# Kernel optimization log

Hardware: AMD Instinct MI355X
Metric: run time of the kernel (lower is better)

Reference implementation:

```python
import jax, jax.numpy as jnp
import numpy as np

N = 500000
V = 50000
GF = 64
OC = 256

def _lin(key, din, dout):
    k1, k2 = jax.random.split(key)
    w = jax.random.normal(k1, (din, dout), dtype=jnp.float32) * 0.02
    b = jax.random.normal(k2, (dout,), dtype=jnp.float32) * 0.02
    return w, b

def setup_inputs() -> dict:
    key = jax.random.key(0)
    ks = jax.random.split(key, 12)
    inp_feat = jax.random.normal(ks[0], (N, 6), dtype=jnp.float32)
    vox2point_idx = jax.random.randint(ks[1], (N,), 0, V, dtype=jnp.int32)
    w1x, b1x = _lin(ks[2], 3, GF)
    w2x, b2x = _lin(ks[3], GF, OC // 8)
    w1r, b1r = _lin(ks[4], 3, GF)
    w2r, b2r = _lin(ks[5], GF, OC // 8)
    wax, bax = _lin(ks[6], OC // 4, OC // 8)
    war, bar = _lin(ks[7], OC // 4, OC // 8)
    wv1, bv1 = _lin(ks[8], OC // 2, OC // 2)
    w3, b3 = _lin(ks[9], OC, OC)
    w4, b4 = _lin(ks[10], OC, OC)
    wv2, bv2 = _lin(ks[11], OC, OC)
    return dict(inp_feat=inp_feat, vox2point_idx=vox2point_idx, num_vox=V,
                w1x=w1x, b1x=b1x, w2x=w2x, b2x=b2x,
                w1r=w1r, b1r=b1r, w2r=w2r, b2r=b2r,
                wax=wax, bax=bax, war=war, bar=bar,
                wv1=wv1, bv1=bv1, w3=w3, b3=b3, w4=w4, b4=b4,
                wv2=wv2, bv2=bv2)

def reference(inp_feat, vox2point_idx, num_vox,
              w1x, b1x, w2x, b2x, w1r, b1r, w2r, b2r,
              wax, bax, war, bar, wv1, bv1, w3, b3, w4, b4, wv2, bv2):
    relu = jax.nn.relu
    xyz = inp_feat[:, :3]
    rgb = inp_feat[:, 3:]
    fx = relu(relu(xyz @ w1x + b1x) @ w2x + b2x)   # [N, 32]
    fr = relu(relu(rgb @ w1r + b1r) @ w2r + b2r)   # [N, 32]
    comb = jnp.concatenate([fx, fr], axis=-1)       # [N, 64]
    pf2 = jnp.concatenate([
        fx, fx * jax.nn.sigmoid(comb @ wax + bax),
        fr, fr * jax.nn.sigmoid(comb @ war + bar)], axis=-1)  # [N, 128]
    # scatter-max to voxels; torch_scatter fills empty segments with 0 and
    # pf2 >= 0 elementwise, so clamp -inf (jax empty fill) to 0 for parity.
    vox = jax.ops.segment_max(pf2, vox2point_idx, num_segments=num_vox)
    vox = jnp.maximum(vox, 0.0)                     # [V, 128]
    vox = relu(vox @ wv1 + bv1)
    pg = vox[vox2point_idx]                          # gather back [N, 128]
    pf3 = jnp.concatenate([pg, pf2], axis=-1)        # [N, 256]
    pf5 = relu(relu(pf3 @ w3 + b3) @ w4 + b4)        # [N, 256]
    vox2 = jax.ops.segment_max(pf5, vox2point_idx, num_segments=num_vox)
    vox2 = jnp.maximum(vox2, 0.0)
    return relu(vox2 @ wv2 + bv2)                    # [V, 256]
```

## Files before the change

kernel.cpp:

```cpp
#include <hip/hip_runtime.h>

#define NPTS 500000
#define NVOX 50000
#define NBLK 196

typedef unsigned short u16;
typedef unsigned int u32;
typedef __attribute__((ext_vector_type(8))) short short8;
typedef __attribute__((ext_vector_type(4))) float floatx4;
typedef __attribute__((ext_vector_type(4))) unsigned int uintx4;

__device__ __forceinline__ u16 f2bf(float f) {
    u32 u = __float_as_uint(f);
    u = u + 0x7fffu + ((u >> 16) & 1u);
    return (u16)(u >> 16);
}

__global__ void k_wtransform(const float* __restrict__ W, u16* __restrict__ Wf, int K, int N) {
    int t = blockIdx.x * 256 + threadIdx.x;
    if (t >= K * N) return;
    int k = t / N, n = t - k * N;
    int kk = k >> 5, q = (k >> 3) & 3, j = k & 7;
    Wf[((size_t)((kk * 4 + q) * N + n) << 3) + j] = f2bf(W[t]);
}

__global__ void k_wcat(const float* __restrict__ w2x, const float* __restrict__ w2r, u16* __restrict__ wcatf) {
    int t = blockIdx.x * 256 + threadIdx.x;
    if (t >= 128 * 64) return;
    int k = t >> 6, n = t & 63;
    float v;
    if (k < 64) v = (n < 32) ? w2x[k * 32 + n] : 0.f;
    else        v = (n >= 32) ? w2r[(k - 64) * 32 + (n - 32)] : 0.f;
    int kk = k >> 5, q = (k >> 3) & 3, j = k & 7;
    wcatf[((size_t)((kk * 4 + q) * 64 + n) << 3) + j] = f2bf(v);
}

__global__ void k_watt(const float* __restrict__ wax, const float* __restrict__ war, u16* __restrict__ wattf) {
    int t = blockIdx.x * 256 + threadIdx.x;
    if (t >= 64 * 64) return;
    int k = t >> 6, n = t & 63;
    float v = (n < 32) ? wax[k * 32 + n] : war[k * 32 + (n - 32)];
    int kk = k >> 5, q = (k >> 3) & 3, j = k & 7;
    wattf[((size_t)((kk * 4 + q) * 64 + n) << 3) + j] = f2bf(v);
}

__global__ void k_hist(const int* __restrict__ idx, int* __restrict__ hcnt) {
    int i = blockIdx.x * 256 + threadIdx.x;
    if (i < NPTS) atomicAdd(&hcnt[idx[i]], 1);
}

__global__ __launch_bounds__(256) void k_scan1(const int* __restrict__ hcnt, int* __restrict__ bsum) {
    __shared__ int wsum[4];
    int t = threadIdx.x;
    int i = blockIdx.x * 256 + t;
    int c = (i < NVOX) ? hcnt[i] : 0;
    #pragma unroll
    for (int d = 32; d >= 1; d >>= 1) c += __shfl_xor(c, d, 64);
    if ((t & 63) == 0) wsum[t >> 6] = c;
    __syncthreads();
    if (t == 0) bsum[blockIdx.x] = wsum[0] + wsum[1] + wsum[2] + wsum[3];
}

__global__ __launch_bounds__(256) void k_scan2(const int* __restrict__ bsum, int* __restrict__ boff) {
    __shared__ int wsum[4];
    int t = threadIdx.x, lane = t & 63, w = t >> 6;
    int c = (t < NBLK) ? bsum[t] : 0;
    int v = c;
    #pragma unroll
    for (int d = 1; d < 64; d <<= 1) {
        int o = __shfl_up(v, d, 64);
        if (lane >= d) v += o;
    }
    if (lane == 63) wsum[w] = v;
    __syncthreads();
    int wo = 0;
    #pragma unroll
    for (int k = 0; k < 4; k++) if (k < w) wo += wsum[k];
    if (t < NBLK) boff[t] = wo + v - c;
}

__global__ __launch_bounds__(256) void k_scan3(const int* __restrict__ hcnt, const int* __restrict__ boff,
                                               int* __restrict__ start, int* __restrict__ cur) {
    __shared__ int wsum[4];
    int t = threadIdx.x, lane = t & 63, w = t >> 6;
    int i = blockIdx.x * 256 + t;
    int c = (i < NVOX) ? hcnt[i] : 0;
    int v = c;
    #pragma unroll
    for (int d = 1; d < 64; d <<= 1) {
        int o = __shfl_up(v, d, 64);
        if (lane >= d) v += o;
    }
    if (lane == 63) wsum[w] = v;
    __syncthreads();
    int wo = 0;
    #pragma unroll
    for (int k = 0; k < 4; k++) if (k < w) wo += wsum[k];
    if (i < NVOX) {
        int excl = boff[blockIdx.x] + wo + v - c;
        start[i] = excl;
        cur[i] = excl;
    }
}

__global__ void k_scatter(const int* __restrict__ idx, int* __restrict__ cur,
                          int* __restrict__ rank, int* __restrict__ svid) {
    int i = blockIdx.x * 256 + threadIdx.x;
    if (i < NPTS) {
        int v = idx[i];
        int pos = atomicAdd(&cur[v], 1);
        rank[i] = pos;
        svid[pos] = v;
    }
}

__global__ __launch_bounds__(256) void k_pointfeat(
    const float* __restrict__ inp, const int* __restrict__ rank,
    const float* __restrict__ w1x, const float* __restrict__ b1x,
    const float* __restrict__ w1r, const float* __restrict__ b1r,
    const u16* __restrict__ wcatf, const float* __restrict__ b2x, const float* __restrict__ b2r,
    const u16* __restrict__ wattf, const float* __restrict__ bax, const float* __restrict__ bar,
    u16* __restrict__ pf2s)
{
    __shared__ u16 hbuf[64 * 136];
    __shared__ u16 cbuf[64 * 72];
    __shared__ float wl[512];
    __shared__ int lrank[64];
    int t = threadIdx.x;
    int i0 = blockIdx.x * 64;
    for (int s = t; s < 512; s += 256) {
        float v;
        if (s < 192)      v = w1x[s];
        else if (s < 256) v = b1x[s - 192];
        else if (s < 448) v = w1r[s - 256];
        else              v = b1r[s - 448];
        wl[s] = v;
    }
    if (t < 64) lrank[t] = (i0 + t < NPTS) ? rank[i0 + t] : 0;
    __syncthreads();
    {
        int m = t >> 2, c = t & 3;
        int i = i0 + m;
        float x0 = 0, x1 = 0, x2 = 0, r0 = 0, r1 = 0, r2 = 0;
        if (i < NPTS) {
            const float* p = inp + (size_t)i * 6;
            x0 = p[0]; x1 = p[1]; x2 = p[2]; r0 = p[3]; r1 = p[4]; r2 = p[5];
        }
        u16* hb = &hbuf[m * 136 + c * 16];
        #pragma unroll
        for (int jp = 0; jp < 8; jp++) {
            int c0 = c * 16 + 2 * jp, c1 = c0 + 1;
            float hx0 = fmaxf(wl[192 + c0] + x0 * wl[c0] + x1 * wl[64 + c0] + x2 * wl[128 + c0], 0.f);
            float hx1 = fmaxf(wl[192 + c1] + x0 * wl[c1] + x1 * wl[64 + c1] + x2 * wl[128 + c1], 0.f);
            float hr0 = fmaxf(wl[448 + c0] + r0 * wl[256 + c0] + r1 * wl[320 + c0] + r2 * wl[384 + c0], 0.f);
            float hr1 = fmaxf(wl[448 + c1] + r0 * wl[256 + c1] + r1 * wl[320 + c1] + r2 * wl[384 + c1], 0.f);
            *(u32*)(hb + 2 * jp)      = (u32)f2bf(hx0) | ((u32)f2bf(hx1) << 16);
            *(u32*)(hb + 64 + 2 * jp) = (u32)f2bf(hr0) | ((u32)f2bf(hr1) << 16);
        }
    }
    __syncthreads();
    int wave = t >> 6, l = t & 63, q = l >> 4, lm = l & 15;
    int n = wave * 16 + lm;
    floatx4 acc[4];
    #pragma unroll
    for (int a = 0; a < 4; a++) acc[a] = (floatx4){0.f, 0.f, 0.f, 0.f};
    #pragma unroll
    for (int kk = 0; kk < 4; kk++) {
        short8 bfrag = *(const short8*)&wcatf[(size_t)((kk * 4 + q) * 64 + n) << 3];
        #pragma unroll
        for (int tm = 0; tm < 4; tm++) {
            short8 afrag = *(const short8*)&hbuf[(tm * 16 + lm) * 136 + kk * 32 + q * 8];
            acc[tm] = __builtin_amdgcn_mfma_f32_16x16x32_bf16(afrag, bfrag, acc[tm], 0, 0, 0);
        }
    }
    float bv = (n < 32) ? b2x[n] : b2r[n - 32];
    float comb_keep[4][4];
    #pragma unroll
    for (int tm = 0; tm < 4; tm++)
        #pragma unroll
        for (int r = 0; r < 4; r++) {
            float v = fmaxf(acc[tm][r] + bv, 0.f);
            comb_keep[tm][r] = v;
            int m = tm * 16 + q * 4 + r;
            cbuf[m * 72 + n] = f2bf(v);
        }
    __syncthreads();
    floatx4 acc2[4];
    #pragma unroll
    for (int a = 0; a < 4; a++) acc2[a] = (floatx4){0.f, 0.f, 0.f, 0.f};
    #pragma unroll
    for (int kk = 0; kk < 2; kk++) {
        short8 bfrag = *(const short8*)&wattf[(size_t)((kk * 4 + q) * 64 + n) << 3];
        #pragma unroll
        for (int tm = 0; tm < 4; tm++) {
            short8 afrag = *(const short8*)&cbuf[(tm * 16 + lm) * 72 + kk * 32 + q * 8];
            acc2[tm] = __builtin_amdgcn_mfma_f32_16x16x32_bf16(afrag, bfrag, acc2[tm], 0, 0, 0);
        }
    }
    float bv2 = (n < 32) ? bax[n] : bar[n - 32];
    int pp = (n < 32) ? n : 32 + n;
    #pragma unroll
    for (int tm = 0; tm < 4; tm++)
        #pragma unroll
        for (int r = 0; r < 4; r++) {
            float att = acc2[tm][r] + bv2;
            float sg = 1.f / (1.f + __expf(-att));
            float plain = comb_keep[tm][r];
            float gated = plain * sg;
            int m = tm * 16 + q * 4 + r;
            hbuf[m * 136 + pp] = f2bf(plain);
            hbuf[m * 136 + pp + 32] = f2bf(gated);
        }
    __syncthreads();
    {
        int row = t >> 2, seg = t & 3;
        if (i0 + row < NPTS) {
            const u16* src = &hbuf[row * 136 + seg * 32];
            u16* dst = pf2s + (size_t)lrank[row] * 128 + seg * 32;
            *(uintx4*)dst = *(const uintx4*)src;
            *(uintx4*)(dst + 8) = *(const uintx4*)(src + 8);
        }
    }
}

__global__ __launch_bounds__(256) void k_segmax(
    const u16* __restrict__ pf2s, const int* __restrict__ start, const int* __restrict__ hcnt,
    u16* __restrict__ voxmax)
{
    int w = threadIdx.x >> 6, l = threadIdx.x & 63;
    int v = blockIdx.x * 4 + w;
    if (v >= NVOX) return;
    int s = start[v], c = hcnt[v];
    const u32* base = (const u32*)pf2s + (size_t)s * 64 + l;
    u32 mlo = 0, mhi = 0;
    for (int e = 0; e < c; e++) {
        u32 u = base[(size_t)e * 64];
        u32 lo = u & 0xffffu, hi = u >> 16;
        mlo = lo > mlo ? lo : mlo;
        mhi = hi > mhi ? hi : mhi;
    }
    ((u32*)voxmax)[(size_t)v * 64 + l] = mlo | (mhi << 16);
}

template<int K, int N, bool ABF16, bool OUT_BF16>
__global__ __launch_bounds__(256) void k_gemm_relu(
    const void* __restrict__ Ap, const u16* __restrict__ Wf,
    const float* __restrict__ bias, void* __restrict__ outp, int M)
{
    constexpr int STRIDE = K + 8;
    constexpr int TN = N / 64;
    constexpr int KSTEPS = K / 32;
    constexpr int CW = K / 4;
    __shared__ u16 lds[64 * STRIDE];
    int i0 = blockIdx.x * 64;
    int mcnt = M - i0; if (mcnt > 64) mcnt = 64;
    int t = threadIdx.x;
    {
        int row = t >> 2, cseg = t & 3;
        u16* dst = &lds[row * STRIDE + cseg * CW];
        if (row < mcnt) {
            if (ABF16) {
                const u16* src = (const u16*)Ap + (size_t)(i0 + row) * K + cseg * CW;
                #pragma unroll
                for (int c = 0; c < CW / 8; c++)
                    *(uintx4*)(dst + c * 8) = *(const uintx4*)(src + c * 8);
            } else {
                const float* src = (const float*)Ap + (size_t)(i0 + row) * K + cseg * CW;
                #pragma unroll
                for (int c = 0; c < CW / 8; c++) {
                    float4 v0 = *(const float4*)(src + c * 8);
                    float4 v1 = *(const float4*)(src + c * 8 + 4);
                    short8 rr;
                    rr[0] = f2bf(v0.x); rr[1] = f2bf(v0.y); rr[2] = f2bf(v0.z); rr[3] = f2bf(v0.w);
                    rr[4] = f2bf(v1.x); rr[5] = f2bf(v1.y); rr[6] = f2bf(v1.z); rr[7] = f2bf(v1.w);
                    *(short8*)(dst + c * 8) = rr;
                }
            }
        } else {
            short8 z = {0, 0, 0, 0, 0, 0, 0, 0};
            #pragma unroll
            for (int c = 0; c < CW / 8; c++) *(short8*)(dst + c * 8) = z;
        }
    }
    __syncthreads();
    int wave = t >> 6, l = t & 63;
    int q = l >> 4, lm = l & 15;
    int wn0 = wave * (N / 4);
    floatx4 acc[4][TN];
    #pragma unroll
    for (int a = 0; a < 4; a++)
        #pragma unroll
        for (int b = 0; b < TN; b++) acc[a][b] = (floatx4){0.f, 0.f, 0.f, 0.f};
    #pragma unroll
    for (int kk = 0; kk < KSTEPS; kk++) {
        short8 afrag[4], bfrag[TN];
        #pragma unroll
        for (int tm = 0; tm < 4; tm++)
            afrag[tm] = *(const short8*)&lds[(tm * 16 + lm) * STRIDE + kk * 32 + q * 8];
        #pragma unroll
        for (int tn = 0; tn < TN; tn++)
            bfrag[tn] = *(const short8*)&Wf[(size_t)((kk * 4 + q) * N + wn0 + tn * 16 + lm) * 8];
        #pragma unroll
        for (int tm = 0; tm < 4; tm++)
            #pragma unroll
            for (int tn = 0; tn < TN; tn++)
                acc[tm][tn] = __builtin_amdgcn_mfma_f32_16x16x32_bf16(afrag[tm], bfrag[tn], acc[tm][tn], 0, 0, 0);
    }
    #pragma unroll
    for (int tm = 0; tm < 4; tm++)
        #pragma unroll
        for (int tn = 0; tn < TN; tn++) {
            int n = wn0 + tn * 16 + lm;
            float bv = bias[n];
            #pragma unroll
            for (int r = 0; r < 4; r++) {
                int m = tm * 16 + q * 4 + r;
                if (m < mcnt) {
                    float v = fmaxf(acc[tm][tn][r] + bv, 0.f);
                    if (OUT_BF16) ((u16*)outp)[(size_t)(i0 + m) * N + n] = f2bf(v);
                    else          ((float*)outp)[(size_t)(i0 + m) * N + n] = v;
                }
            }
        }
}

__global__ __launch_bounds__(256) void k_pointmlp(
    const u16* __restrict__ voxf, const u16* __restrict__ pf2s, const int* __restrict__ svid,
    const u16* __restrict__ w3f, const float* __restrict__ b3,
    const u16* __restrict__ w4f, const float* __restrict__ b4,
    float* __restrict__ vox2)
{
    constexpr int STRIDE = 264;
    __shared__ u16 lds[64 * STRIDE];
    __shared__ int lvid[64];
    int i0 = blockIdx.x * 64;
    int mcnt = NPTS - i0; if (mcnt > 64) mcnt = 64;
    int t = threadIdx.x;
    if (t < 64) lvid[t] = (t < mcnt) ? svid[i0 + t] : -1;
    {
        int row = t >> 2, cseg = t & 3;
        u16* dst = &lds[row * STRIDE + cseg * 64];
        if (row < mcnt) {
            const u16* src;
            if (cseg < 2) src = voxf + (size_t)svid[i0 + row] * 128 + cseg * 64;
            else          src = pf2s + (size_t)(i0 + row) * 128 + (cseg - 2) * 64;
            #pragma unroll
            for (int c = 0; c < 8; c++)
                *(uintx4*)(dst + c * 8) = *(const uintx4*)(src + c * 8);
        } else {
            uintx4 z = {0, 0, 0, 0};
            #pragma unroll
            for (int c = 0; c < 8; c++) *(uintx4*)(dst + c * 8) = z;
        }
    }
    __syncthreads();
    int wave = t >> 6, l = t & 63;
    int q = l >> 4, lm = l & 15;
    int wn0 = wave * 64;
    floatx4 acc[4][4];
    #pragma unroll
    for (int a = 0; a < 4; a++)
        #pragma unroll
        for (int b = 0; b < 4; b++) acc[a][b] = (floatx4){0.f, 0.f, 0.f, 0.f};
    #pragma unroll
    for (int kk = 0; kk < 8; kk++) {
        short8 afrag[4], bfrag[4];
        #pragma unroll
        for (int tm = 0; tm < 4; tm++)
            afrag[tm] = *(const short8*)&lds[(tm * 16 + lm) * STRIDE + kk * 32 + q * 8];
        #pragma unroll
        for (int tn = 0; tn < 4; tn++)
            bfrag[tn] = *(const short8*)&w3f[(size_t)((kk * 4 + q) * 256 + wn0 + tn * 16 + lm) * 8];
        #pragma unroll
        for (int tm = 0; tm < 4; tm++)
            #pragma unroll
            for (int tn = 0; tn < 4; tn++)
                acc[tm][tn] = __builtin_amdgcn_mfma_f32_16x16x32_bf16(afrag[tm], bfrag[tn], acc[tm][tn], 0, 0, 0);
    }
    __syncthreads();
    #pragma unroll
    for (int tm = 0; tm < 4; tm++)
        #pragma unroll
        for (int tn = 0; tn < 4; tn++) {
            int n = wn0 + tn * 16 + lm;
            float bv = b3[n];
            #pragma unroll
            for (int r = 0; r < 4; r++) {
                int m = tm * 16 + q * 4 + r;
                lds[m * STRIDE + n] = f2bf(fmaxf(acc[tm][tn][r] + bv, 0.f));
            }
        }
    __syncthreads();
    floatx4 acc2[4][4];
    #pragma unroll
    for (int a = 0; a < 4; a++)
        #pragma unroll
        for (int b = 0; b < 4; b++) acc2[a][b] = (floatx4){0.f, 0.f, 0.f, 0.f};
    #pragma unroll
    for (int kk = 0; kk < 8; kk++) {
        short8 afrag[4], bfrag[4];
        #pragma unroll
        for (int tm = 0; tm < 4; tm++)
            afrag[tm] = *(const short8*)&lds[(tm * 16 + lm) * STRIDE + kk * 32 + q * 8];
        #pragma unroll
        for (int tn = 0; tn < 4; tn++)
            bfrag[tn] = *(const short8*)&w4f[(size_t)((kk * 4 + q) * 256 + wn0 + tn * 16 + lm) * 8];
        #pragma unroll
        for (int tm = 0; tm < 4; tm++)
            #pragma unroll
            for (int tn = 0; tn < 4; tn++)
                acc2[tm][tn] = __builtin_amdgcn_mfma_f32_16x16x32_bf16(afrag[tm], bfrag[tn], acc2[tm][tn], 0, 0, 0);
    }
    __syncthreads();
    #pragma unroll
    for (int tm = 0; tm < 4; tm++)
        #pragma unroll
        for (int tn = 0; tn < 4; tn++) {
            int n = wn0 + tn * 16 + lm;
            float bv = b4[n];
            #pragma unroll
            for (int r = 0; r < 4; r++) {
                int m = tm * 16 + q * 4 + r;
                lds[m * STRIDE + n] = f2bf(fmaxf(acc2[tm][tn][r] + bv, 0.f));
            }
        }
    __syncthreads();
    {
        int c2 = t & 127;
        int h = t >> 7;
        int r0 = h * 32;
        int r1 = r0 + 32; if (r1 > mcnt) r1 = mcnt;
        u32 mlo = 0, mhi = 0;
        int pvid = -1;
        for (int r = r0; r < r1; r++) {
            int vid = lvid[r];
            if (vid != pvid) {
                if (pvid >= 0) {
                    int* addr = (int*)(vox2 + (size_t)pvid * 256 + 2 * c2);
                    if (mlo) atomicMax(addr, (int)(mlo << 16));
                    if (mhi) atomicMax(addr + 1, (int)(mhi << 16));
                }
                pvid = vid; mlo = 0; mhi = 0;
            }
            u32 u = *(const u32*)&lds[r * STRIDE + 2 * c2];
            u32 lo = u & 0xffffu, hi = u >> 16;
            mlo = lo > mlo ? lo : mlo;
            mhi = hi > mhi ? hi : mhi;
        }
        if (pvid >= 0) {
            int* addr = (int*)(vox2 + (size_t)pvid * 256 + 2 * c2);
            if (mlo) atomicMax(addr, (int)(mlo << 16));
            if (mhi) atomicMax(addr + 1, (int)(mhi << 16));
        }
    }
}

extern "C" void kernel_launch(void* const* d_in, const int* in_sizes, int n_in,
                              void* d_out, int out_size, void* d_ws, size_t ws_size,
                              hipStream_t stream) {
    const float* inp = (const float*)d_in[0];
    const int*   idx = (const int*)d_in[1];
    const float* w1x = (const float*)d_in[3];  const float* b1x = (const float*)d_in[4];
    const float* w2x = (const float*)d_in[5];  const float* b2x = (const float*)d_in[6];
    const float* w1r = (const float*)d_in[7];  const float* b1r = (const float*)d_in[8];
    const float* w2r = (const float*)d_in[9];  const float* b2r = (const float*)d_in[10];
    const float* wax = (const float*)d_in[11]; const float* bax = (const float*)d_in[12];
    const float* war = (const float*)d_in[13]; const float* bar = (const float*)d_in[14];
    const float* wv1 = (const float*)d_in[15]; const float* bv1 = (const float*)d_in[16];
    const float* w3  = (const float*)d_in[17]; const float* b3  = (const float*)d_in[18];
    const float* w4  = (const float*)d_in[19]; const float* b4  = (const float*)d_in[20];
    const float* wv2 = (const float*)d_in[21]; const float* bv2 = (const float*)d_in[22];
    float* out = (float*)d_out;

    char* ws = (char*)d_ws;
    u16*   pf2s   = (u16*)ws;   ws += (size_t)NPTS * 128 * sizeof(u16);
    u16*   voxmax = (u16*)ws;   ws += (size_t)NVOX * 128 * sizeof(u16);
    u16*   voxf   = (u16*)ws;   ws += (size_t)NVOX * 128 * sizeof(u16);
    float* vox2   = (float*)ws; ws += (size_t)NVOX * 256 * sizeof(float);
    u16*   w3f    = (u16*)ws;   ws += 65536 * sizeof(u16);
    u16*   w4f    = (u16*)ws;   ws += 65536 * sizeof(u16);
    u16*   wv1f   = (u16*)ws;   ws += 16384 * sizeof(u16);
    u16*   wv2f   = (u16*)ws;   ws += 65536 * sizeof(u16);
    u16*   wcatf  = (u16*)ws;   ws += 8192 * sizeof(u16);
    u16*   wattf  = (u16*)ws;   ws += 4096 * sizeof(u16);
    int*   hcnt   = (int*)ws;   ws += (size_t)NVOX * sizeof(int);
    int*   start  = (int*)ws;   ws += (size_t)NVOX * sizeof(int);
    int*   cur    = (int*)ws;   ws += (size_t)NVOX * sizeof(int);
    int*   bsum   = (int*)ws;   ws += (size_t)NBLK * sizeof(int);
    int*   boff   = (int*)ws;   ws += (size_t)NBLK * sizeof(int);
    int*   rank   = (int*)ws;   ws += (size_t)NPTS * sizeof(int);
    int*   svid   = (int*)ws;   ws += (size_t)NPTS * sizeof(int);

    hipMemsetAsync(hcnt, 0, (size_t)NVOX * sizeof(int), stream);
    hipMemsetAsync(vox2, 0, (size_t)NVOX * 256 * sizeof(float), stream);

    k_wtransform<<<256, 256, 0, stream>>>(w3, w3f, 256, 256);
    k_wtransform<<<256, 256, 0, stream>>>(w4, w4f, 256, 256);
    k_wtransform<<<64,  256, 0, stream>>>(wv1, wv1f, 128, 128);
    k_wtransform<<<256, 256, 0, stream>>>(wv2, wv2f, 256, 256);
    k_wcat<<<32, 256, 0, stream>>>(w2x, w2r, wcatf);
    k_watt<<<16, 256, 0, stream>>>(wax, war, wattf);

    k_hist<<<(NPTS + 255) / 256, 256, 0, stream>>>(idx, hcnt);
    k_scan1<<<NBLK, 256, 0, stream>>>(hcnt, bsum);
    k_scan2<<<1, 256, 0, stream>>>(bsum, boff);
    k_scan3<<<NBLK, 256, 0, stream>>>(hcnt, boff, start, cur);
    k_scatter<<<(NPTS + 255) / 256, 256, 0, stream>>>(idx, cur, rank, svid);

    k_pointfeat<<<(NPTS + 63) / 64, 256, 0, stream>>>(
        inp, rank, w1x, b1x, w1r, b1r, wcatf, b2x, b2r, wattf, bax, bar, pf2s);

    k_segmax<<<(NVOX + 3) / 4, 256, 0, stream>>>(pf2s, start, hcnt, voxmax);

    k_gemm_relu<128, 128, true, true><<<(NVOX + 63) / 64, 256, 0, stream>>>(
        (const void*)voxmax, wv1f, bv1, (void*)voxf, NVOX);

    k_pointmlp<<<(NPTS + 63) / 64, 256, 0, stream>>>(
        voxf, pf2s, svid, w3f, b3, w4f, b4, vox2);

    k_gemm_relu<256, 256, false, false><<<(NVOX + 63) / 64, 256, 0, stream>>>(
        (const void*)vox2, wv2f, bv2, (void*)out, NVOX);
}
```

Measured before the change: 524.1 us.

## Fuse voxel segment-max into pointfeat via sorted-order processing and atomics

Points are now processed in voxel-sorted order: scatter records each point's original id, pointfeat gathers inputs through it and writes pf2 contiguously. Pointfeat also does a run-length max over consecutive same-voxel rows in LDS and issues float atomicMax into an fp32 voxmax buffer, so the separate segmax kernel and the start array go away. The pointmlp GEMMs swap operand roles so each result row is packed into vectorized LDS writes, with biases staged in shared memory. This adds an extra memset and global atomics and doubles voxmax storage, but removes a full re-read of pf2s.

```diff
diff --git a/kernel.cpp b/kernel.cpp
--- a/kernel.cpp
+++ b/kernel.cpp
@@ -9,6 +9,7 @@
 typedef __attribute__((ext_vector_type(8))) short short8;
 typedef __attribute__((ext_vector_type(4))) float floatx4;
 typedef __attribute__((ext_vector_type(4))) unsigned int uintx4;
+typedef __attribute__((ext_vector_type(2))) unsigned int uintx2;
 
 __device__ __forceinline__ u16 f2bf(float f) {
     u32 u = __float_as_uint(f);
@@ -80,7 +81,7 @@
 }
 
 __global__ __launch_bounds__(256) void k_scan3(const int* __restrict__ hcnt, const int* __restrict__ boff,
-                                               int* __restrict__ start, int* __restrict__ cur) {
+                                               int* __restrict__ cur) {
     __shared__ int wsum[4];
     int t = threadIdx.x, lane = t & 63, w = t >> 6;
     int i = blockIdx.x * 256 + t;
@@ -96,38 +97,35 @@
     int wo = 0;
     #pragma unroll
     for (int k = 0; k < 4; k++) if (k < w) wo += wsum[k];
-    if (i < NVOX) {
-        int excl = boff[blockIdx.x] + wo + v - c;
-        start[i] = excl;
-        cur[i] = excl;
-    }
+    if (i < NVOX) cur[i] = boff[blockIdx.x] + wo + v - c;
 }
 
 __global__ void k_scatter(const int* __restrict__ idx, int* __restrict__ cur,
-                          int* __restrict__ rank, int* __restrict__ svid) {
+                          int* __restrict__ sptid, int* __restrict__ svid) {
     int i = blockIdx.x * 256 + threadIdx.x;
     if (i < NPTS) {
         int v = idx[i];
         int pos = atomicAdd(&cur[v], 1);
-        rank[i] = pos;
+        sptid[pos] = i;
         svid[pos] = v;
     }
 }
 
 __global__ __launch_bounds__(256) void k_pointfeat(
-    const float* __restrict__ inp, const int* __restrict__ rank,
+    const float* __restrict__ inp, const int* __restrict__ sptid, const int* __restrict__ svid,
     const float* __restrict__ w1x, const float* __restrict__ b1x,
     const float* __restrict__ w1r, const float* __restrict__ b1r,
     const u16* __restrict__ wcatf, const float* __restrict__ b2x, const float* __restrict__ b2r,
     const u16* __restrict__ wattf, const float* __restrict__ bax, const float* __restrict__ bar,
-    u16* __restrict__ pf2s)
+    u16* __restrict__ pf2s, float* __restrict__ voxmax)
 {
     __shared__ u16 hbuf[64 * 136];
     __shared__ u16 cbuf[64 * 72];
     __shared__ float wl[512];
-    __shared__ int lrank[64];
+    __shared__ int lvid[64];
     int t = threadIdx.x;
     int i0 = blockIdx.x * 64;
+    int mcnt = NPTS - i0; if (mcnt > 64) mcnt = 64;
     for (int s = t; s < 512; s += 256) {
         float v;
         if (s < 192)      v = w1x[s];
@@ -136,14 +134,13 @@
         else              v = b1r[s - 448];
         wl[s] = v;
     }
-    if (t < 64) lrank[t] = (i0 + t < NPTS) ? rank[i0 + t] : 0;
+    if (t < 64) lvid[t] = (t < mcnt) ? svid[i0 + t] : -1;
     __syncthreads();
     {
         int m = t >> 2, c = t & 3;
-        int i = i0 + m;
         float x0 = 0, x1 = 0, x2 = 0, r0 = 0, r1 = 0, r2 = 0;
-        if (i < NPTS) {
-            const float* p = inp + (size_t)i * 6;
+        if (m < mcnt) {
+            const float* p = inp + (size_t)sptid[i0 + m] * 6;
             x0 = p[0]; x1 = p[1]; x2 = p[2]; r0 = p[3]; r1 = p[4]; r2 = p[5];
         }
         u16* hb = &hbuf[m * 136 + c * 16];
@@ -214,32 +211,41 @@
     __syncthreads();
     {
         int row = t >> 2, seg = t & 3;
-        if (i0 + row < NPTS) {
+        if (row < mcnt) {
             const u16* src = &hbuf[row * 136 + seg * 32];
-            u16* dst = pf2s + (size_t)lrank[row] * 128 + seg * 32;
+            u16* dst = pf2s + (size_t)(i0 + row) * 128 + seg * 32;
             *(uintx4*)dst = *(const uintx4*)src;
             *(uintx4*)(dst + 8) = *(const uintx4*)(src + 8);
         }
     }
-}
-
-__global__ __launch_bounds__(256) void k_segmax(
-    const u16* __restrict__ pf2s, const int* __restrict__ start, const int* __restrict__ hcnt,
-    u16* __restrict__ voxmax)
-{
-    int w = threadIdx.x >> 6, l = threadIdx.x & 63;
-    int v = blockIdx.x * 4 + w;
-    if (v >= NVOX) return;
-    int s = start[v], c = hcnt[v];
-    const u32* base = (const u32*)pf2s + (size_t)s * 64 + l;
-    u32 mlo = 0, mhi = 0;
-    for (int e = 0; e < c; e++) {
-        u32 u = base[(size_t)e * 64];
-        u32 lo = u & 0xffffu, hi = u >> 16;
-        mlo = lo > mlo ? lo : mlo;
-        mhi = hi > mhi ? hi : mhi;
-    }
-    ((u32*)voxmax)[(size_t)v * 64 + l] = mlo | (mhi << 16);
+    {
+        int c2 = t & 63;
+        int h = t >> 6;
+        int r0 = h * 16;
+        int r1 = r0 + 16; if (r1 > mcnt) r1 = mcnt;
+        u32 mlo = 0, mhi = 0;
+        int pvid = -1;
+        for (int r = r0; r < r1; r++) {
+            int vid = lvid[r];
+            if (vid != pvid) {
+                if (pvid >= 0) {
+                    int* addr = (int*)(voxmax + (size_t)pvid * 128 + 2 * c2);
+                    if (mlo) atomicMax(addr, (int)(mlo << 16));
+                    if (mhi) atomicMax(addr + 1, (int)(mhi << 16));
+                }
+                pvid = vid; mlo = 0; mhi = 0;
+            }
+            u32 u = *(const u32*)&hbuf[r * 136 + 2 * c2];
+            u32 lo = u & 0xffffu, hi = u >> 16;
+            mlo = lo > mlo ? lo : mlo;
+            mhi = hi > mhi ? hi : mhi;
+        }
+        if (pvid >= 0) {
+            int* addr = (int*)(voxmax + (size_t)pvid * 128 + 2 * c2);
+            if (mlo) atomicMax(addr, (int)(mlo << 16));
+            if (mhi) atomicMax(addr + 1, (int)(mhi << 16));
+        }
+    }
 }
 
 template<int K, int N, bool ABF16, bool OUT_BF16>
@@ -333,10 +339,12 @@
     constexpr int STRIDE = 264;
     __shared__ u16 lds[64 * STRIDE];
     __shared__ int lvid[64];
+    __shared__ float bl[512];
     int i0 = blockIdx.x * 64;
     int mcnt = NPTS - i0; if (mcnt > 64) mcnt = 64;
     int t = threadIdx.x;
     if (t < 64) lvid[t] = (t < mcnt) ? svid[i0 + t] : -1;
+    for (int s = t; s < 512; s += 256) bl[s] = (s < 256) ? b3[s] : b4[s - 256];
     {
         int row = t >> 2, cseg = t & 3;
         u16* dst = &lds[row * STRIDE + cseg * 64];
@@ -356,7 +364,7 @@
     __syncthreads();
     int wave = t >> 6, l = t & 63;
     int q = l >> 4, lm = l & 15;
-    int wn0 = wave * 64;
+    int wm0 = wave * 64;
     floatx4 acc[4][4];
     #pragma unroll
     for (int a = 0; a < 4; a++)
@@ -364,32 +372,30 @@
         for (int b = 0; b < 4; b++) acc[a][b] = (floatx4){0.f, 0.f, 0.f, 0.f};
     #pragma unroll
     for (int kk = 0; kk < 8; kk++) {
-        short8 afrag[4], bfrag[4];
+        short8 wfrag[4], bfrag[4];
         #pragma unroll
         for (int tm = 0; tm < 4; tm++)
-            afrag[tm] = *(const short8*)&lds[(tm * 16 + lm) * STRIDE + kk * 32 + q * 8];
+            wfrag[tm] = *(const short8*)&w3f[(size_t)((kk * 4 + q) * 256 + wm0 + tm * 16 + lm) * 8];
         #pragma unroll
         for (int tn = 0; tn < 4; tn++)
-            bfrag[tn] = *(const short8*)&w3f[(size_t)((kk * 4 + q) * 256 + wn0 + tn * 16 + lm) * 8];
+            bfrag[tn] = *(const short8*)&lds[(tn * 16 + lm) * STRIDE + kk * 32 + q * 8];
         #pragma unroll
         for (int tm = 0; tm < 4; tm++)
             #pragma unroll
             for (int tn = 0; tn < 4; tn++)
-                acc[tm][tn] = __builtin_amdgcn_mfma_f32_16x16x32_bf16(afrag[tm], bfrag[tn], acc[tm][tn], 0, 0, 0);
-    }
-    __syncthreads();
-    #pragma unroll
-    for (int tm = 0; tm < 4; tm++)
+                acc[tm][tn] = __builtin_amdgcn_mfma_f32_16x16x32_bf16(wfrag[tm], bfrag[tn], acc[tm][tn], 0, 0, 0);
+    }
+    __syncthreads();
+    #pragma unroll
+    for (int tm = 0; tm < 4; tm++) {
+        float4 bq = *(const float4*)&bl[wm0 + tm * 16 + 4 * q];
         #pragma unroll
         for (int tn = 0; tn < 4; tn++) {
-            int n = wn0 + tn * 16 + lm;
-            float bv = b3[n];
-            #pragma unroll
-            for (int r = 0; r < 4; r++) {
-                int m = tm * 16 + q * 4 + r;
-                lds[m * STRIDE + n] = f2bf(fmaxf(acc[tm][tn][r] + bv, 0.f));
-            }
-        }
+            u32 lo = (u32)f2bf(fmaxf(acc[tm][tn][0] + bq.x, 0.f)) | ((u32)f2bf(fmaxf(acc[tm][tn][1] + bq.y, 0.f)) << 16);
+            u32 hi = (u32)f2bf(fmaxf(acc[tm][tn][2] + bq.z, 0.f)) | ((u32)f2bf(fmaxf(acc[tm][tn][3] + bq.w, 0.f)) << 16);
+            *(uintx2*)&lds[(tn * 16 + lm) * STRIDE + wm0 + tm * 16 + 4 * q] = (uintx2){lo, hi};
+        }
+    }
     __syncthreads();
     floatx4 acc2[4][4];
     #pragma unroll
@@ -398,32 +404,30 @@
         for (int b = 0; b < 4; b++) acc2[a][b] = (floatx4){0.f, 0.f, 0.f, 0.f};
     #pragma unroll
     for (int kk = 0; kk < 8; kk++) {
-        short8 afrag[4], bfrag[4];
+        short8 wfrag[4], bfrag[4];
         #pragma unroll
         for (int tm = 0; tm < 4; tm++)
-            afrag[tm] = *(const short8*)&lds[(tm * 16 + lm) * STRIDE + kk * 32 + q * 8];
+            wfrag[tm] = *(const short8*)&w4f[(size_t)((kk * 4 + q) * 256 + wm0 + tm * 16 + lm) * 8];
         #pragma unroll
         for (int tn = 0; tn < 4; tn++)
-            bfrag[tn] = *(const short8*)&w4f[(size_t)((kk * 4 + q) * 256 + wn0 + tn * 16 + lm) * 8];
+            bfrag[tn] = *(const short8*)&lds[(tn * 16 + lm) * STRIDE + kk * 32 + q * 8];
         #pragma unroll
         for (int tm = 0; tm < 4; tm++)
             #pragma unroll
             for (int tn = 0; tn < 4; tn++)
-                acc2[tm][tn] = __builtin_amdgcn_mfma_f32_16x16x32_bf16(afrag[tm], bfrag[tn], acc2[tm][tn], 0, 0, 0);
-    }
-    __syncthreads();
-    #pragma unroll
-    for (int tm = 0; tm < 4; tm++)
+                acc2[tm][tn] = __builtin_amdgcn_mfma_f32_16x16x32_bf16(wfrag[tm], bfrag[tn], acc2[tm][tn], 0, 0, 0);
+    }
+    __syncthreads();
+    #pragma unroll
+    for (int tm = 0; tm < 4; tm++) {
+        float4 bq = *(const float4*)&bl[256 + wm0 + tm * 16 + 4 * q];
         #pragma unroll
         for (int tn = 0; tn < 4; tn++) {
-            int n = wn0 + tn * 16 + lm;
-            float bv = b4[n];
-            #pragma unroll
-            for (int r = 0; r < 4; r++) {
-                int m = tm * 16 + q * 4 + r;
-                lds[m * STRIDE + n] = f2bf(fmaxf(acc2[tm][tn][r] + bv, 0.f));
-            }
-        }
+            u32 lo = (u32)f2bf(fmaxf(acc2[tm][tn][0] + bq.x, 0.f)) | ((u32)f2bf(fmaxf(acc2[tm][tn][1] + bq.y, 0.f)) << 16);
+            u32 hi = (u32)f2bf(fmaxf(acc2[tm][tn][2] + bq.z, 0.f)) | ((u32)f2bf(fmaxf(acc2[tm][tn][3] + bq.w, 0.f)) << 16);
+            *(uintx2*)&lds[(tn * 16 + lm) * STRIDE + wm0 + tm * 16 + 4 * q] = (uintx2){lo, hi};
+        }
+    }
     __syncthreads();
     {
         int c2 = t & 127;
@@ -474,7 +478,7 @@
 
     char* ws = (char*)d_ws;
     u16*   pf2s   = (u16*)ws;   ws += (size_t)NPTS * 128 * sizeof(u16);
-    u16*   voxmax = (u16*)ws;   ws += (size_t)NVOX * 128 * sizeof(u16);
+    float* voxmax = (float*)ws; ws += (size_t)NVOX * 128 * sizeof(float);
     u16*   voxf   = (u16*)ws;   ws += (size_t)NVOX * 128 * sizeof(u16);
     float* vox2   = (float*)ws; ws += (size_t)NVOX * 256 * sizeof(float);
     u16*   w3f    = (u16*)ws;   ws += 65536 * sizeof(u16);
@@ -484,14 +488,14 @@
     u16*   wcatf  = (u16*)ws;   ws += 8192 * sizeof(u16);
     u16*   wattf  = (u16*)ws;   ws += 4096 * sizeof(u16);
     int*   hcnt   = (int*)ws;   ws += (size_t)NVOX * sizeof(int);
-    int*   start  = (int*)ws;   ws += (size_t)NVOX * sizeof(int);
     int*   cur    = (int*)ws;   ws += (size_t)NVOX * sizeof(int);
     int*   bsum   = (int*)ws;   ws += (size_t)NBLK * sizeof(int);
     int*   boff   = (int*)ws;   ws += (size_t)NBLK * sizeof(int);
-    int*   rank   = (int*)ws;   ws += (size_t)NPTS * sizeof(int);
+    int*   sptid  = (int*)ws;   ws += (size_t)NPTS * sizeof(int);
     int*   svid   = (int*)ws;   ws += (size_t)NPTS * sizeof(int);
 
     hipMemsetAsync(hcnt, 0, (size_t)NVOX * sizeof(int), stream);
+    hipMemsetAsync(voxmax, 0, (size_t)NVOX * 128 * sizeof(float), stream);
     hipMemsetAsync(vox2, 0, (size_t)NVOX * 256 * sizeof(float), stream);
 
     k_wtransform<<<256, 256, 0, stream>>>(w3, w3f, 256, 256);
@@ -504,15 +508,13 @@
     k_hist<<<(NPTS + 255) / 256, 256, 0, stream>>>(idx, hcnt);
     k_scan1<<<NBLK, 256, 0, stream>>>(hcnt, bsum);
     k_scan2<<<1, 256, 0, stream>>>(bsum, boff);
-    k_scan3<<<NBLK, 256, 0, stream>>>(hcnt, boff, start, cur);
-    k_scatter<<<(NPTS + 255) / 256, 256, 0, stream>>>(idx, cur, rank, svid);
+    k_scan3<<<NBLK, 256, 0, stream>>>(hcnt, boff, cur);
+    k_scatter<<<(NPTS + 255) / 256, 256, 0, stream>>>(idx, cur, sptid, svid);
 
     k_pointfeat<<<(NPTS + 63) / 64, 256, 0, stream>>>(
-        inp, rank, w1x, b1x, w1r, b1r, wcatf, b2x, b2r, wattf, bax, bar, pf2s);
-
-    k_segmax<<<(NVOX + 3) / 4, 256, 0, stream>>>(pf2s, start, hcnt, voxmax);
-
-    k_gemm_relu<128, 128, true, true><<<(NVOX + 63) / 64, 256, 0, stream>>>(
+        inp, sptid, svid, w1x, b1x, w1r, b1r, wcatf, b2x, b2r, wattf, bax, bar, pf2s, voxmax);
+
+    k_gemm_relu<128, 128, false, true><<<(NVOX + 63) / 64, 256, 0, stream>>>(
         (const void*)voxmax, wv1f, bv1, (void*)voxf, NVOX);
 
     k_pointmlp<<<(NPTS + 63) / 64, 256, 0, stream>>>(
```

Result: faster. 493.7 us (-5.8%).
